# Optimization experiments

Hardware: AMD Instinct MI355X
Metric: run time of the kernel (lower is better)

Reference implementation:

```python
import jax, jax.numpy as jnp
import numpy as np

B, N, C = 4, 16384, 512
HEADS = 16
HEADC = C // HEADS
HIDDEN = int(C * 4.0)


def setup_inputs() -> dict:
    key = jax.random.key(0)
    ks = jax.random.split(key, 8)
    s1 = 1.0 / np.sqrt(C)
    s2 = 1.0 / np.sqrt(HIDDEN)
    return {
        "x": jax.random.normal(ks[0], (B, N, C), jnp.float32),
        "mask_matrix": jnp.zeros((1,), jnp.int32),
        "norm1_w": jnp.ones((C,), jnp.float32),
        "norm1_b": jnp.zeros((C,), jnp.float32),
        "kln_w": jnp.ones((HEADS, 1, HEADC), jnp.float32),
        "kln_b": jnp.zeros((HEADS, 1, HEADC), jnp.float32),
        "vln_w": jnp.ones((HEADS, 1, HEADC), jnp.float32),
        "vln_b": jnp.zeros((HEADS, 1, HEADC), jnp.float32),
        "norm2_w": jnp.ones((C,), jnp.float32),
        "norm2_b": jnp.zeros((C,), jnp.float32),
        "fc1_w": jax.random.uniform(ks[1], (HIDDEN, C), jnp.float32, -s1, s1),
        "fc1_b": jax.random.uniform(ks[2], (HIDDEN,), jnp.float32, -s1, s1),
        "fc2_w": jax.random.uniform(ks[3], (C, HIDDEN), jnp.float32, -s2, s2),
        "fc2_b": jax.random.uniform(ks[4], (C,), jnp.float32, -s2, s2),
    }


def _ln(t, w, b, eps=1e-5):
    # standard nn.LayerNorm: biased variance, eps inside sqrt
    mean = t.mean(-1, keepdims=True)
    var = ((t - mean) ** 2).mean(-1, keepdims=True)
    return w * (t - mean) / jnp.sqrt(var + eps) + b


def _ln_std(t, w, b, eps=1e-5):
    # custom LayerNorm: unbiased std (torch.std), eps added to std
    d = t.shape[-1]
    mean = t.mean(-1, keepdims=True)
    var = ((t - mean) ** 2).sum(-1, keepdims=True) / (d - 1)
    return w * ((t - mean) / (jnp.sqrt(var) + eps)) + b


def reference(x, mask_matrix, norm1_w, norm1_b, kln_w, kln_b, vln_w, vln_b,
              norm2_w, norm2_b, fc1_w, fc1_b, fc2_w, fc2_b):
    b, n, c = x.shape
    shortcut = x
    h = _ln(x, norm1_w, norm1_b)
    # simple_attn (softmax-free linear attention)
    qkv = h.reshape(b, n, HEADS, HEADC).transpose(0, 2, 1, 3)  # [B,H,N,D]
    q = qkv
    k = _ln_std(qkv, kln_w, kln_b)
    v = _ln_std(qkv, vln_w, vln_b)
    kv = jnp.einsum('bhnd,bhne->bhde', k, v) / n        # [B,H,D,D]
    attn = jnp.einsum('bhnd,bhde->bhne', q, kv)          # [B,H,N,D]
    attn = attn.transpose(0, 2, 1, 3).reshape(b, n, c)
    h = attn + h                                          # residual inside simple_attn (bias = x post-norm1)
    x = shortcut + h
    # MLP branch
    m = _ln(x, norm2_w, norm2_b)
    m = jax.nn.gelu(m @ fc1_w.T + fc1_b, approximate=False)
    m = m @ fc2_w.T + fc2_b
    return x + m
```

## Files before the change

kernel.cpp:

```cpp
#include <hip/hip_runtime.h>
#include <cstdint>

#define BB 4
#define NN 16384
#define CC 512
#define HH 16
#define DD 32
#define HID 2048
#define MTOT (BB * NN)

typedef __bf16 bf16_t;
typedef __bf16 bf16x8 __attribute__((ext_vector_type(8)));
typedef __bf16 bf16x4 __attribute__((ext_vector_type(4)));
typedef float  f32x4  __attribute__((ext_vector_type(4)));

__device__ __forceinline__ void gload_lds16(const void* g, void* l) {
  auto gp = reinterpret_cast<const __attribute__((address_space(1))) char*>(
      reinterpret_cast<uintptr_t>(g));
  auto lp = reinterpret_cast<__attribute__((address_space(3))) char*>(
      reinterpret_cast<uintptr_t>(l));
  __builtin_amdgcn_global_load_lds(gp, lp, 16, 0, 0);
}

__global__ __launch_bounds__(256) void cvt_bf16_kernel(const float* __restrict__ src,
                                                       bf16_t* __restrict__ dst) {
  const long i = ((long)blockIdx.x * 256 + threadIdx.x) * 4;
  const f32x4 v = *(const f32x4*)(src + i);
  bf16x4 o;
  o[0] = (bf16_t)v[0]; o[1] = (bf16_t)v[1]; o[2] = (bf16_t)v[2]; o[3] = (bf16_t)v[3];
  *(bf16x4*)(dst + i) = o;
}

__global__ __launch_bounds__(256) void norm1_kernel(const float* __restrict__ x,
                                                    const float* __restrict__ w,
                                                    const float* __restrict__ bvec,
                                                    bf16_t* __restrict__ h) {
  const int wv = threadIdx.x >> 6, l = threadIdx.x & 63;
  const long tok = (long)blockIdx.x * 4 + wv;
  const int c0 = l * 8;
  const f32x4 a = *(const f32x4*)(x + tok * CC + c0);
  const f32x4 b = *(const f32x4*)(x + tok * CC + c0 + 4);
  float v[8];
#pragma unroll
  for (int i = 0; i < 4; ++i) { v[i] = a[i]; v[4 + i] = b[i]; }
  float s = 0.f, s2 = 0.f;
#pragma unroll
  for (int i = 0; i < 8; ++i) { s += v[i]; s2 += v[i] * v[i]; }
  for (int off = 32; off; off >>= 1) { s += __shfl_xor(s, off); s2 += __shfl_xor(s2, off); }
  const float mean = s * (1.f / CC);
  const float var  = fmaxf(s2 * (1.f / CC) - mean * mean, 0.f);
  const float rstd = rsqrtf(var + 1e-5f);
  const f32x4 w0 = *(const f32x4*)(w + c0), w1 = *(const f32x4*)(w + c0 + 4);
  const f32x4 b0 = *(const f32x4*)(bvec + c0), b1 = *(const f32x4*)(bvec + c0 + 4);
  bf16x8 o;
#pragma unroll
  for (int i = 0; i < 4; ++i) {
    o[i]     = (bf16_t)(w0[i] * (v[i] - mean) * rstd + b0[i]);
    o[4 + i] = (bf16_t)(w1[i] * (v[4 + i] - mean) * rstd + b1[i]);
  }
  *(bf16x8*)(h + tok * CC + c0) = o;
}

__global__ __launch_bounds__(256) void kv_partial_kernel(const bf16_t* __restrict__ h,
                                                         const float* __restrict__ klw,
                                                         const float* __restrict__ klb,
                                                         const float* __restrict__ vlw,
                                                         const float* __restrict__ vlb,
                                                         float* __restrict__ kvp) {
  __shared__ bf16_t kb[256 * 32];
  __shared__ bf16_t vb[256 * 32];
  __shared__ float scratch[192 * 16];
  const int tid = threadIdx.x;
  const int bh = blockIdx.x >> 6, chunk = blockIdx.x & 63;
  const int head = bh & 15;
  const int b = bh >> 4;
  const long tok0 = ((long)b << 14) + chunk * 256;
  const bf16_t* src = h + (tok0 + tid) * (long)CC + head * DD;
  float hv[32];
  {
    float s = 0.f, s2 = 0.f;
#pragma unroll
    for (int c = 0; c < 4; ++c) {
      const bf16x8 r = *(const bf16x8*)(src + c * 8);
#pragma unroll
      for (int j = 0; j < 8; ++j) {
        hv[c * 8 + j] = (float)r[j]; s += hv[c * 8 + j]; s2 += hv[c * 8 + j] * hv[c * 8 + j];
      }
    }
    const float mean = s * (1.f / 32.f);
    const float varu = fmaxf((s2 - 32.f * mean * mean) * (1.f / 31.f), 0.f);
    const float inv = 1.f / (sqrtf(varu) + 1e-5f);
    const int sx = (tid >> 1) & 3;
#pragma unroll
    for (int c = 0; c < 4; ++c) {
      bf16x8 kc, vc;
#pragma unroll
      for (int j = 0; j < 8; ++j) {
        const int d = c * 8 + j;
        const float t = (hv[d] - mean) * inv;
        kc[j] = (bf16_t)(klw[head * DD + d] * t + klb[head * DD + d]);
        vc[j] = (bf16_t)(vlw[head * DD + d] * t + vlb[head * DD + d]);
      }
      *(bf16x8*)((char*)kb + tid * 64 + ((c ^ sx) * 16)) = kc;
      *(bf16x8*)((char*)vb + tid * 64 + ((c ^ sx) * 16)) = vc;
    }
  }
  __syncthreads();
  const int g = tid >> 6, l = tid & 63;
  const int d0 = (l >> 3) * 4, e0 = (l & 7) * 4;
  const int ck = (l >> 3) >> 1, hk = (l >> 3) & 1;
  const int ce = (l & 7) >> 1, he = l & 1;
  float a[4][4] = {};
  for (int t = g; t < 256; t += 4) {
    const int tx = (t >> 1) & 3;
    const bf16x4 kq = *(const bf16x4*)((const char*)kb + t * 64 + ((ck ^ tx) * 16) + hk * 8);
    const bf16x4 vq = *(const bf16x4*)((const char*)vb + t * 64 + ((ce ^ tx) * 16) + he * 8);
    float kf[4], vf[4];
#pragma unroll
    for (int i2 = 0; i2 < 4; ++i2) { kf[i2] = (float)kq[i2]; vf[i2] = (float)vq[i2]; }
#pragma unroll
    for (int i2 = 0; i2 < 4; ++i2)
#pragma unroll
      for (int j2 = 0; j2 < 4; ++j2) a[i2][j2] += kf[i2] * vf[j2];
  }
  __syncthreads();
  if (g) {
#pragma unroll
    for (int i2 = 0; i2 < 4; ++i2)
#pragma unroll
      for (int j2 = 0; j2 < 4; ++j2)
        scratch[((g - 1) * 64 + l) * 16 + i2 * 4 + j2] = a[i2][j2];
  }
  __syncthreads();
  if (!g) {
#pragma unroll
    for (int gg = 0; gg < 3; ++gg)
#pragma unroll
      for (int i2 = 0; i2 < 4; ++i2)
#pragma unroll
        for (int j2 = 0; j2 < 4; ++j2)
          a[i2][j2] += scratch[(gg * 64 + l) * 16 + i2 * 4 + j2];
    float* dst = kvp + ((long)(bh * 64 + chunk) << 10);
#pragma unroll
    for (int i2 = 0; i2 < 4; ++i2) {
      f32x4 st;
      st[0] = a[i2][0]; st[1] = a[i2][1]; st[2] = a[i2][2]; st[3] = a[i2][3];
      *(f32x4*)&dst[(d0 + i2) * 32 + e0] = st;
    }
  }
}

__global__ __launch_bounds__(256) void kv_reduce_kernel(const float* __restrict__ kvp,
                                                        bf16_t* __restrict__ kvT) {
  const int bh = blockIdx.x;
  const int i4 = threadIdx.x * 4;
  const int d = i4 >> 5, e0 = i4 & 31;
  float s[4] = {};
  const float* p = kvp + ((long)bh << 16) + i4;
  for (int ch = 0; ch < 64; ++ch) {
    const f32x4 t = *(const f32x4*)(p + (ch << 10));
    s[0] += t[0]; s[1] += t[1]; s[2] += t[2]; s[3] += t[3];
  }
  const float sc = 1.f / (float)NN;
  bf16_t* q = kvT + ((long)bh << 10);
#pragma unroll
  for (int j = 0; j < 4; ++j) q[(e0 + j) * 32 + d] = (bf16_t)(s[j] * sc);
}

#define ASTRIDE 520
__global__ __launch_bounds__(256) void attn_fused_kernel(const float* __restrict__ x,
                                                         const bf16_t* __restrict__ h,
                                                         const bf16_t* __restrict__ kvTg,
                                                         const float* __restrict__ n2w,
                                                         const float* __restrict__ n2b,
                                                         float* __restrict__ xout,
                                                         bf16_t* __restrict__ mout) {
  __shared__ bf16_t attn_s[32 * ASTRIDE];
  const int tid = threadIdx.x;
  const int wv = tid >> 6, lane = tid & 63;
  const int lr = lane & 15, kg = lane >> 4;
  const long tok0 = (long)blockIdx.x * 32;
  const int b = (int)(tok0 >> 14);
  const bf16_t* kvsrc = kvTg + ((long)b << 14);

  {
    const int tt = wv & 1, hh = wv >> 1;
    const bf16_t* arow = h + (tok0 + tt * 16 + lr) * (long)CC + kg * 8;
    const f32x4 zero = {};
#pragma unroll
    for (int hi = 0; hi < 8; ++hi) {
      const int hd = hh * 8 + hi;
      const bf16_t* kvh = kvsrc + (hd << 10) + kg * 8;
      const bf16x8 af = *(const bf16x8*)(arow + hd * DD);
      const bf16x8 b0 = *(const bf16x8*)(kvh + lr * 32);
      const bf16x8 b1 = *(const bf16x8*)(kvh + (16 + lr) * 32);
      const f32x4 a0 = __builtin_amdgcn_mfma_f32_16x16x32_bf16(af, b0, zero, 0, 0, 0);
      const f32x4 a1 = __builtin_amdgcn_mfma_f32_16x16x32_bf16(af, b1, zero, 0, 0, 0);
      const int rbase = tt * 16 + kg * 4;
#pragma unroll
      for (int rg = 0; rg < 4; ++rg) {
        attn_s[(rbase + rg) * ASTRIDE + hd * 32 + lr]      = (bf16_t)a0[rg];
        attn_s[(rbase + rg) * ASTRIDE + hd * 32 + 16 + lr] = (bf16_t)a1[rg];
      }
    }
  }
  __syncthreads();

  const int c0 = lane * 8;
  const f32x4 w0 = *(const f32x4*)(n2w + c0), w1 = *(const f32x4*)(n2w + c0 + 4);
  const f32x4 bb0 = *(const f32x4*)(n2b + c0), bb1 = *(const f32x4*)(n2b + c0 + 4);
  for (int it = 0; it < 8; ++it) {
    const int tl = wv * 8 + it;
    const long tok = tok0 + tl;
    const f32x4 xa = *(const f32x4*)(x + tok * CC + c0);
    const f32x4 xb = *(const f32x4*)(x + tok * CC + c0 + 4);
    const bf16x8 hv = *(const bf16x8*)(h + tok * CC + c0);
    const bf16x8 av = *(const bf16x8*)&attn_s[tl * ASTRIDE + c0];
    float x2[8];
#pragma unroll
    for (int i = 0; i < 4; ++i) {
      x2[i]     = xa[i] + (float)hv[i]     + (float)av[i];
      x2[4 + i] = xb[i] + (float)hv[4 + i] + (float)av[4 + i];
    }
    float s = 0.f, s2 = 0.f;
#pragma unroll
    for (int i = 0; i < 8; ++i) { s += x2[i]; s2 += x2[i] * x2[i]; }
    for (int off = 32; off; off >>= 1) { s += __shfl_xor(s, off); s2 += __shfl_xor(s2, off); }
    const float mean = s * (1.f / CC);
    const float var  = fmaxf(s2 * (1.f / CC) - mean * mean, 0.f);
    const float rstd = rsqrtf(var + 1e-5f);
    f32x4 oa, ob;
    bf16x8 om;
#pragma unroll
    for (int i = 0; i < 4; ++i) {
      oa[i] = x2[i]; ob[i] = x2[4 + i];
      om[i]     = (bf16_t)(w0[i] * (x2[i] - mean) * rstd + bb0[i]);
      om[4 + i] = (bf16_t)(w1[i] * (x2[4 + i] - mean) * rstd + bb1[i]);
    }
    *(f32x4*)(xout + tok * CC + c0) = oa;
    *(f32x4*)(xout + tok * CC + c0 + 4) = ob;
    *(bf16x8*)(mout + tok * CC + c0) = om;
  }
}

template <int K, int NOUT, bool GELU>
__global__ __launch_bounds__(256, 3) void gemm97_kernel(const bf16_t* __restrict__ A,
                                                        const bf16_t* __restrict__ Bw,
                                                        const float* __restrict__ bias,
                                                        bf16_t* __restrict__ outb,
                                                        float* __restrict__ outf) {
  constexpr int NTILE = NOUT / 128;
  constexpr int NT = K / 32;
  __shared__ char lds[32768];
  char* As = lds;
  char* Bs = lds + 8192;

  const int tid = threadIdx.x;
  const int wid = tid >> 6, lane = tid & 63;
  const int wr = wid >> 1, wc = wid & 1;
  const int lr = lane & 15, kg = lane >> 4;

  int bid = blockIdx.x;
  const int qq = gridDim.x >> 3;
  bid = (bid & 7) * qq + (bid >> 3);
  const long row0 = (long)(bid / NTILE) * 128;
  const long col0 = (long)(bid % NTILE) * 128;

  const int srow = tid >> 2;
  const int sce = (((tid & 3) ^ ((srow >> 1) & 3)) << 3);
  const bf16_t* gA = A + (row0 + srow) * (long)K + sce;
  const bf16_t* gB = Bw + (col0 + srow) * (long)K + sce;

  f32x4 acc[4][4] = {};

  const int cx = ((kg ^ ((lr >> 1) & 3)) << 4);
  const char* aB = As + (wr * 64 + lr) * 64 + cx;
  const char* bB = Bs + (wc * 64 + lr) * 64 + cx;

  for (int kt = 0; kt < NT; ++kt) {
    gload_lds16(gA + kt * 32, As + tid * 16);
    gload_lds16(gA + 64L * K + kt * 32, As + 4096 + tid * 16);
    gload_lds16(gB + kt * 32, Bs + tid * 16);
    gload_lds16(gB + 64L * K + kt * 32, Bs + 4096 + tid * 16);
    __syncthreads();
    bf16x8 af[4], bf[4];
#pragma unroll
    for (int m = 0; m < 4; ++m) af[m] = *(const bf16x8*)(aB + m * 1024);
#pragma unroll
    for (int n = 0; n < 4; ++n) bf[n] = *(const bf16x8*)(bB + n * 1024);
#pragma unroll
    for (int m = 0; m < 4; ++m)
#pragma unroll
      for (int n = 0; n < 4; ++n)
        acc[m][n] = __builtin_amdgcn_mfma_f32_16x16x32_bf16(af[m], bf[n], acc[m][n], 0, 0, 0);
    __syncthreads();
  }

  if constexpr (GELU) {
    bf16_t* ot = (bf16_t*)lds;
#pragma unroll
    for (int n = 0; n < 4; ++n) {
      const int col = wc * 64 + n * 16 + lr;
      const float bs = bias[col0 + col];
#pragma unroll
      for (int m = 0; m < 4; ++m) {
#pragma unroll
        for (int rg = 0; rg < 4; ++rg) {
          const int row = wr * 64 + m * 16 + kg * 4 + rg;
          const float v = acc[m][n][rg] + bs;
          const float u = 0.7978845608028654f * (v + 0.044715f * v * v * v);
          const float gv = v / (1.f + __expf(-2.f * u));
          const int ch = (col >> 3) ^ ((row >> 2) & 3);
          ot[row * 128 + ch * 8 + (col & 7)] = (bf16_t)gv;
        }
      }
    }
    __syncthreads();
#pragma unroll
    for (int it2 = 0; it2 < 8; ++it2) {
      const int idx = it2 * 256 + tid;
      const int row = idx >> 4, ch = idx & 15;
      const int chs = ch ^ ((row >> 2) & 3);
      const bf16x8 vv = *(const bf16x8*)&ot[row * 128 + chs * 8];
      *(bf16x8*)(outb + (row0 + row) * NOUT + col0 + ch * 8) = vv;
    }
  } else {
#pragma unroll
    for (int n = 0; n < 4; ++n) {
      const long col = col0 + wc * 64 + n * 16 + lr;
      const float bs = bias[col];
#pragma unroll
      for (int m = 0; m < 4; ++m) {
#pragma unroll
        for (int rg = 0; rg < 4; ++rg) {
          const long row = row0 + wr * 64 + m * 16 + kg * 4 + rg;
          outf[row * NOUT + col] += acc[m][n][rg] + bs;
        }
      }
    }
  }
}

extern "C" void kernel_launch(void* const* d_in, const int* in_sizes, int n_in,
                              void* d_out, int out_size, void* d_ws, size_t ws_size,
                              hipStream_t stream) {
  const float* x   = (const float*)d_in[0];
  const float* n1w = (const float*)d_in[2];
  const float* n1b = (const float*)d_in[3];
  const float* klw = (const float*)d_in[4];
  const float* klb = (const float*)d_in[5];
  const float* vlw = (const float*)d_in[6];
  const float* vlb = (const float*)d_in[7];
  const float* n2w = (const float*)d_in[8];
  const float* n2b = (const float*)d_in[9];
  const float* w1f = (const float*)d_in[10];
  const float* b1  = (const float*)d_in[11];
  const float* w2f = (const float*)d_in[12];
  const float* b2  = (const float*)d_in[13];
  float* out = (float*)d_out;

  int nch;
  if (ws_size >= 289538048ULL) nch = 2;
  else                         nch = 4;
  const long mch = MTOT / nch;

  char* ws = (char*)d_ws;
  size_t off = 0;
  bf16_t* h   = (bf16_t*)(ws + off); off += (size_t)MTOT * CC * 2;
  bf16_t* mb  = (bf16_t*)(ws + off); off += (size_t)MTOT * CC * 2;
  bf16_t* act = (bf16_t*)(ws + off); off += (size_t)mch * HID * 2;
  bf16_t* w1  = (bf16_t*)(ws + off); off += (size_t)HID * CC * 2;
  bf16_t* w2  = (bf16_t*)(ws + off); off += (size_t)HID * CC * 2;
  float*  kvp = (float*)(ws + off);  off += (size_t)BB * HH * 64 * 1024 * 4;
  bf16_t* kvT = (bf16_t*)(ws + off);

  cvt_bf16_kernel<<<1024, 256, 0, stream>>>(w1f, w1);
  cvt_bf16_kernel<<<1024, 256, 0, stream>>>(w2f, w2);
  norm1_kernel<<<MTOT / 4, 256, 0, stream>>>(x, n1w, n1b, h);
  kv_partial_kernel<<<BB * HH * 64, 256, 0, stream>>>(h, klw, klb, vlw, vlb, kvp);
  kv_reduce_kernel<<<BB * HH, 256, 0, stream>>>(kvp, kvT);
  attn_fused_kernel<<<MTOT / 32, 256, 0, stream>>>(x, h, kvT, n2w, n2b, out, mb);
  for (int ch = 0; ch < nch; ++ch) {
    gemm97_kernel<CC, HID, true>
        <<<(int)((mch / 128) * (HID / 128)), 256, 0, stream>>>(
        mb + (size_t)ch * mch * CC, w1, b1, act, nullptr);
    gemm97_kernel<HID, CC, false>
        <<<(int)((mch / 128) * (CC / 128)), 256, 0, stream>>>(
        act, w2, b2, nullptr, out + (size_t)ch * mch * CC);
  }
}
```

Measured before the change: 663.0 us.

## Rewrite MLP GEMMs with per-wave double-buffered 32x32 MFMA and bf16 residual

The shared-LDS, barrier-synchronised GEMM is replaced by a per-wave private-LDS kernel. Each wave double-buffers its own 64x64 tile with async global-to-LDS loads, explicit vmcnt waits and 32x32x16 MFMAs, which removes block-level barriers from the K loop. The attention kernel now stores the post-attention residual as bf16 instead of fp32 and software-prefetches the next token's x and h. The fc2 epilogue writes out = x2b + result instead of doing a read-modify-write on fp32. Storing the residual in bf16 loses precision, the epilogue stores are uncoalesced scalar writes, and an extra workspace buffer is required.

```diff
diff --git a/kernel.cpp b/kernel.cpp
--- a/kernel.cpp
+++ b/kernel.cpp
@@ -13,6 +13,7 @@
 typedef __bf16 bf16x8 __attribute__((ext_vector_type(8)));
 typedef __bf16 bf16x4 __attribute__((ext_vector_type(4)));
 typedef float  f32x4  __attribute__((ext_vector_type(4)));
+typedef float  f32x16 __attribute__((ext_vector_type(16)));
 
 __device__ __forceinline__ void gload_lds16(const void* g, void* l) {
   auto gp = reinterpret_cast<const __attribute__((address_space(1))) char*>(
@@ -173,7 +174,7 @@
                                                          const bf16_t* __restrict__ kvTg,
                                                          const float* __restrict__ n2w,
                                                          const float* __restrict__ n2b,
-                                                         float* __restrict__ xout,
+                                                         bf16_t* __restrict__ x2b,
                                                          bf16_t* __restrict__ mout) {
   __shared__ bf16_t attn_s[32 * ASTRIDE];
   const int tid = threadIdx.x;
@@ -204,17 +205,28 @@
       }
     }
   }
-  __syncthreads();
 
   const int c0 = lane * 8;
   const f32x4 w0 = *(const f32x4*)(n2w + c0), w1 = *(const f32x4*)(n2w + c0 + 4);
   const f32x4 bb0 = *(const f32x4*)(n2b + c0), bb1 = *(const f32x4*)(n2b + c0 + 4);
+
+  const long tokp = tok0 + wv * 8;
+  f32x4 xa = *(const f32x4*)(x + tokp * CC + c0);
+  f32x4 xb = *(const f32x4*)(x + tokp * CC + c0 + 4);
+  bf16x8 hv = *(const bf16x8*)(h + tokp * CC + c0);
+  __syncthreads();
+
+#pragma unroll
   for (int it = 0; it < 8; ++it) {
     const int tl = wv * 8 + it;
     const long tok = tok0 + tl;
-    const f32x4 xa = *(const f32x4*)(x + tok * CC + c0);
-    const f32x4 xb = *(const f32x4*)(x + tok * CC + c0 + 4);
-    const bf16x8 hv = *(const bf16x8*)(h + tok * CC + c0);
+    f32x4 xa1, xb1;
+    bf16x8 hv1;
+    if (it < 7) {
+      xa1 = *(const f32x4*)(x + (tok + 1) * CC + c0);
+      xb1 = *(const f32x4*)(x + (tok + 1) * CC + c0 + 4);
+      hv1 = *(const bf16x8*)(h + (tok + 1) * CC + c0);
+    }
     const bf16x8 av = *(const bf16x8*)&attn_s[tl * ASTRIDE + c0];
     float x2[8];
 #pragma unroll
@@ -229,112 +241,122 @@
     const float mean = s * (1.f / CC);
     const float var  = fmaxf(s2 * (1.f / CC) - mean * mean, 0.f);
     const float rstd = rsqrtf(var + 1e-5f);
-    f32x4 oa, ob;
-    bf16x8 om;
+    bf16x8 ox, om;
 #pragma unroll
     for (int i = 0; i < 4; ++i) {
-      oa[i] = x2[i]; ob[i] = x2[4 + i];
+      ox[i]     = (bf16_t)x2[i];
+      ox[4 + i] = (bf16_t)x2[4 + i];
       om[i]     = (bf16_t)(w0[i] * (x2[i] - mean) * rstd + bb0[i]);
       om[4 + i] = (bf16_t)(w1[i] * (x2[4 + i] - mean) * rstd + bb1[i]);
     }
-    *(f32x4*)(xout + tok * CC + c0) = oa;
-    *(f32x4*)(xout + tok * CC + c0 + 4) = ob;
+    *(bf16x8*)(x2b + tok * CC + c0) = ox;
     *(bf16x8*)(mout + tok * CC + c0) = om;
+    xa = xa1; xb = xb1; hv = hv1;
   }
 }
 
 template <int K, int NOUT, bool GELU>
-__global__ __launch_bounds__(256, 3) void gemm97_kernel(const bf16_t* __restrict__ A,
-                                                        const bf16_t* __restrict__ Bw,
-                                                        const float* __restrict__ bias,
-                                                        bf16_t* __restrict__ outb,
-                                                        float* __restrict__ outf) {
+__global__ __launch_bounds__(256, 2) void gemm_wp_kernel(const bf16_t* __restrict__ A,
+                                                         const bf16_t* __restrict__ Bw,
+                                                         const float* __restrict__ bias,
+                                                         bf16_t* __restrict__ outb,
+                                                         float* __restrict__ outf,
+                                                         const bf16_t* __restrict__ x2b) {
+  constexpr int NT = K / 32;
   constexpr int NTILE = NOUT / 128;
-  constexpr int NT = K / 32;
-  __shared__ char lds[32768];
-  char* As = lds;
-  char* Bs = lds + 8192;
+  __shared__ char lds[4 * 16384];
 
   const int tid = threadIdx.x;
   const int wid = tid >> 6, lane = tid & 63;
-  const int wr = wid >> 1, wc = wid & 1;
-  const int lr = lane & 15, kg = lane >> 4;
+  const int wm = wid >> 1, wn = wid & 1;
+  const int l31 = lane & 31, kg5 = lane >> 5;
 
   int bid = blockIdx.x;
   const int qq = gridDim.x >> 3;
   bid = (bid & 7) * qq + (bid >> 3);
-  const long row0 = (long)(bid / NTILE) * 128;
-  const long col0 = (long)(bid % NTILE) * 128;
-
-  const int srow = tid >> 2;
-  const int sce = (((tid & 3) ^ ((srow >> 1) & 3)) << 3);
-  const bf16_t* gA = A + (row0 + srow) * (long)K + sce;
-  const bf16_t* gB = Bw + (col0 + srow) * (long)K + sce;
-
-  f32x4 acc[4][4] = {};
-
-  const int cx = ((kg ^ ((lr >> 1) & 3)) << 4);
-  const char* aB = As + (wr * 64 + lr) * 64 + cx;
-  const char* bB = Bs + (wc * 64 + lr) * 64 + cx;
+  const long row0 = (long)(bid / NTILE) * 128 + wm * 64;
+  const long col0 = (long)(bid % NTILE) * 128 + wn * 64;
+
+  char* ldsw = (char*)lds + wid * 16384;
+  const bf16_t* gA = A + row0 * (long)K;
+  const bf16_t* gB = Bw + col0 * (long)K;
+
+  const int sr = lane >> 2, sc = lane & 3;
+
+  auto STAGE = [&](int buf, int kt) {
+    char* dA = ldsw + buf * 8192 + lane * 16;
+    char* dB = dA + 4096;
+#pragma unroll
+    for (int j = 0; j < 4; ++j) {
+      const int rj = j * 16 + sr;
+      const int swzj = ((rj >> 1) & 3) ^ ((rj >> 3) & 3);
+      const int ce = ((sc ^ swzj) << 3);
+      gload_lds16(gA + (long)rj * K + kt * 32 + ce, dA + j * 1024);
+      gload_lds16(gB + (long)rj * K + kt * 32 + ce, dB + j * 1024);
+    }
+  };
+
+  f32x16 acc[2][2] = {};
+  bf16x8 af[4], bf[4];
+
+  const int swz = ((l31 >> 1) & 3) ^ ((l31 >> 3) & 3);
+  const int cb0 = (((0 << 1) | kg5) ^ swz) << 4;
+  const int cb1 = (((1 << 1) | kg5) ^ swz) << 4;
+
+  auto RDALL = [&](int buf) {
+    const char* a_ = ldsw + buf * 8192 + l31 * 64;
+    const char* b_ = a_ + 4096;
+    af[0] = *(const bf16x8*)(a_ + cb0);
+    af[1] = *(const bf16x8*)(a_ + 2048 + cb0);
+    af[2] = *(const bf16x8*)(a_ + cb1);
+    af[3] = *(const bf16x8*)(a_ + 2048 + cb1);
+    bf[0] = *(const bf16x8*)(b_ + cb0);
+    bf[1] = *(const bf16x8*)(b_ + 2048 + cb0);
+    bf[2] = *(const bf16x8*)(b_ + cb1);
+    bf[3] = *(const bf16x8*)(b_ + 2048 + cb1);
+  };
+
+  STAGE(0, 0);
+  if (NT > 1) STAGE(1, 1);
 
   for (int kt = 0; kt < NT; ++kt) {
-    gload_lds16(gA + kt * 32, As + tid * 16);
-    gload_lds16(gA + 64L * K + kt * 32, As + 4096 + tid * 16);
-    gload_lds16(gB + kt * 32, Bs + tid * 16);
-    gload_lds16(gB + 64L * K + kt * 32, Bs + 4096 + tid * 16);
-    __syncthreads();
-    bf16x8 af[4], bf[4];
-#pragma unroll
-    for (int m = 0; m < 4; ++m) af[m] = *(const bf16x8*)(aB + m * 1024);
-#pragma unroll
-    for (int n = 0; n < 4; ++n) bf[n] = *(const bf16x8*)(bB + n * 1024);
-#pragma unroll
-    for (int m = 0; m < 4; ++m)
-#pragma unroll
-      for (int n = 0; n < 4; ++n)
-        acc[m][n] = __builtin_amdgcn_mfma_f32_16x16x32_bf16(af[m], bf[n], acc[m][n], 0, 0, 0);
-    __syncthreads();
-  }
-
-  if constexpr (GELU) {
-    bf16_t* ot = (bf16_t*)lds;
-#pragma unroll
-    for (int n = 0; n < 4; ++n) {
-      const int col = wc * 64 + n * 16 + lr;
-      const float bs = bias[col0 + col];
-#pragma unroll
-      for (int m = 0; m < 4; ++m) {
-#pragma unroll
-        for (int rg = 0; rg < 4; ++rg) {
-          const int row = wr * 64 + m * 16 + kg * 4 + rg;
-          const float v = acc[m][n][rg] + bs;
+    const int buf = kt & 1;
+    if (kt == NT - 1) asm volatile("s_waitcnt vmcnt(0)" ::: "memory");
+    else              asm volatile("s_waitcnt vmcnt(8)" ::: "memory");
+    RDALL(buf);
+    asm volatile("s_waitcnt lgkmcnt(0)" ::: "memory");
+    __builtin_amdgcn_sched_barrier(0);
+    if (kt + 2 < NT) STAGE(buf, kt + 2);
+    __builtin_amdgcn_s_setprio(1);
+#pragma unroll
+    for (int mf = 0; mf < 2; ++mf)
+#pragma unroll
+      for (int nf = 0; nf < 2; ++nf)
+        acc[mf][nf] = __builtin_amdgcn_mfma_f32_32x32x16_bf16(af[mf], bf[nf], acc[mf][nf], 0, 0, 0);
+#pragma unroll
+    for (int mf = 0; mf < 2; ++mf)
+#pragma unroll
+      for (int nf = 0; nf < 2; ++nf)
+        acc[mf][nf] = __builtin_amdgcn_mfma_f32_32x32x16_bf16(af[2 + mf], bf[2 + nf], acc[mf][nf], 0, 0, 0);
+    __builtin_amdgcn_s_setprio(0);
+  }
+
+#pragma unroll
+  for (int mf = 0; mf < 2; ++mf) {
+#pragma unroll
+    for (int nf = 0; nf < 2; ++nf) {
+      const long col = col0 + nf * 32 + l31;
+      const float bs = bias[col];
+#pragma unroll
+      for (int r = 0; r < 16; ++r) {
+        const long row = row0 + mf * 32 + (r & 3) + 8 * (r >> 2) + 4 * kg5;
+        const float v = acc[mf][nf][r] + bs;
+        if constexpr (GELU) {
           const float u = 0.7978845608028654f * (v + 0.044715f * v * v * v);
           const float gv = v / (1.f + __expf(-2.f * u));
-          const int ch = (col >> 3) ^ ((row >> 2) & 3);
-          ot[row * 128 + ch * 8 + (col & 7)] = (bf16_t)gv;
-        }
-      }
-    }
-    __syncthreads();
-#pragma unroll
-    for (int it2 = 0; it2 < 8; ++it2) {
-      const int idx = it2 * 256 + tid;
-      const int row = idx >> 4, ch = idx & 15;
-      const int chs = ch ^ ((row >> 2) & 3);
-      const bf16x8 vv = *(const bf16x8*)&ot[row * 128 + chs * 8];
-      *(bf16x8*)(outb + (row0 + row) * NOUT + col0 + ch * 8) = vv;
-    }
-  } else {
-#pragma unroll
-    for (int n = 0; n < 4; ++n) {
-      const long col = col0 + wc * 64 + n * 16 + lr;
-      const float bs = bias[col];
-#pragma unroll
-      for (int m = 0; m < 4; ++m) {
-#pragma unroll
-        for (int rg = 0; rg < 4; ++rg) {
-          const long row = row0 + wr * 64 + m * 16 + kg * 4 + rg;
-          outf[row * NOUT + col] += acc[m][n][rg] + bs;
+          outb[row * NOUT + col] = (bf16_t)gv;
+        } else {
+          outf[row * NOUT + col] = (float)x2b[row * NOUT + col] + v;
         }
       }
     }
@@ -360,7 +382,7 @@
   float* out = (float*)d_out;
 
   int nch;
-  if (ws_size >= 289538048ULL) nch = 2;
+  if (ws_size >= 360000000ULL) nch = 2;
   else                         nch = 4;
   const long mch = MTOT / nch;
 
@@ -368,6 +390,7 @@
   size_t off = 0;
   bf16_t* h   = (bf16_t*)(ws + off); off += (size_t)MTOT * CC * 2;
   bf16_t* mb  = (bf16_t*)(ws + off); off += (size_t)MTOT * CC * 2;
+  bf16_t* x2b = (bf16_t*)(ws + off); off += (size_t)MTOT * CC * 2;
   bf16_t* act = (bf16_t*)(ws + off); off += (size_t)mch * HID * 2;
   bf16_t* w1  = (bf16_t*)(ws + off); off += (size_t)HID * CC * 2;
   bf16_t* w2  = (bf16_t*)(ws + off); off += (size_t)HID * CC * 2;
@@ -379,13 +402,14 @@
   norm1_kernel<<<MTOT / 4, 256, 0, stream>>>(x, n1w, n1b, h);
   kv_partial_kernel<<<BB * HH * 64, 256, 0, stream>>>(h, klw, klb, vlw, vlb, kvp);
   kv_reduce_kernel<<<BB * HH, 256, 0, stream>>>(kvp, kvT);
-  attn_fused_kernel<<<MTOT / 32, 256, 0, stream>>>(x, h, kvT, n2w, n2b, out, mb);
+  attn_fused_kernel<<<MTOT / 32, 256, 0, stream>>>(x, h, kvT, n2w, n2b, x2b, mb);
   for (int ch = 0; ch < nch; ++ch) {
-    gemm97_kernel<CC, HID, true>
+    gemm_wp_kernel<CC, HID, true>
         <<<(int)((mch / 128) * (HID / 128)), 256, 0, stream>>>(
-        mb + (size_t)ch * mch * CC, w1, b1, act, nullptr);
-    gemm97_kernel<HID, CC, false>
+        mb + (size_t)ch * mch * CC, w1, b1, act, nullptr, nullptr);
+    gemm_wp_kernel<HID, CC, false>
         <<<(int)((mch / 128) * (CC / 128)), 256, 0, stream>>>(
-        act, w2, b2, nullptr, out + (size_t)ch * mch * CC);
-  }
-}
+        act, w2, b2, nullptr, out + (size_t)ch * mch * CC,
+        x2b + (size_t)ch * mch * CC);
+  }
+}
```

Result: slower. 747.7 us (+12.8%).
